# Optimization experiments

Measured on AMD Instinct MI355X. Metric: run time of the kernel, lower is better.

Reference implementation:

```python
import jax, jax.numpy as jnp
import numpy as np

N, D_IN, D_HID, D_OUT = 100000, 128, 512, 256
EPS = 1e-5


def _kaiming_uniform(k, shape):
    # torch kaiming_uniform_(a=sqrt(5)) -> bound = sqrt(1/fan_in)
    fan_in = shape[1]
    bound = float(np.sqrt(1.0 / fan_in))
    return jax.random.uniform(k, shape, minval=-bound, maxval=bound, dtype=jnp.float32)


def setup_inputs() -> dict:
    key = jax.random.key(0)
    ks = jax.random.split(key, 10)
    in_set = jax.random.normal(ks[0], (N, D_IN), dtype=jnp.float32)
    matA0 = _kaiming_uniform(ks[1], (D_HID, D_IN))
    matB0 = _kaiming_uniform(ks[2], (D_HID, D_IN))
    matA1 = _kaiming_uniform(ks[3], (D_HID, D_HID))
    matB1 = _kaiming_uniform(ks[4], (D_HID, D_HID))
    matA2 = _kaiming_uniform(ks[5], (D_HID, D_HID))
    matB2 = _kaiming_uniform(ks[6], (D_HID, D_HID))
    ln_gamma = jnp.ones((D_HID,), dtype=jnp.float32)
    ln_beta = jnp.zeros((D_HID,), dtype=jnp.float32)
    out_bound = float(np.sqrt(1.0 / D_HID))
    out_w = jax.random.uniform(ks[7], (D_OUT, D_HID), minval=-out_bound, maxval=out_bound, dtype=jnp.float32)
    out_b = jax.random.uniform(ks[8], (D_OUT,), minval=-out_bound, maxval=out_bound, dtype=jnp.float32)
    return {"in_set": in_set, "matA0": matA0, "matB0": matB0, "matA1": matA1, "matB1": matB1,
            "matA2": matA2, "matB2": matB2, "ln_gamma": ln_gamma, "ln_beta": ln_beta,
            "out_w": out_w, "out_b": out_b}


def _layer(h, A, B, g, b):
    # f(x_i) = relu(LN(A x_i + B (sum_j x_j - x_i)))
    # vectorized: h @ (A-B)^T + total_sum @ B^T  (sum-minus-self identity)
    s = h.sum(axis=0)  # [d]
    h = h @ (A - B).T + s @ B.T  # [N, d_hid]
    mu = h.mean(axis=-1, keepdims=True)
    var = jnp.mean((h - mu) ** 2, axis=-1, keepdims=True)
    h = (h - mu) / jnp.sqrt(var + EPS) * g + b
    return jax.nn.relu(h)


def reference(in_set, matA0, matB0, matA1, matB1, matA2, matB2, ln_gamma, ln_beta, out_w, out_b):
    h = _layer(in_set, matA0, matB0, ln_gamma, ln_beta)
    h = _layer(h, matA1, matB1, ln_gamma, ln_beta)
    h = _layer(h, matA2, matB2, ln_gamma, ln_beta)
    h = h.max(axis=0)  # max-pool over set elements -> [d_hid]
    return h @ out_w.T + out_b  # [d_out]
```

## Files before the change

kernel.cpp:

```cpp
#include <hip/hip_runtime.h>
#include <hip/hip_bf16.h>

#define NPTS 100000
#define NPTS_PAD 100096
#define DHID 512
#define EPSV 1e-5f

typedef __attribute__((ext_vector_type(4))) float f32x4;

#define OFF_INBF   0UL
#define OFF_W0     12812288UL
#define OFF_W1     12877824UL
#define OFF_W2     13139968UL
#define OFF_C0     13402112UL
#define OFF_C1     13404160UL
#define OFF_C2     13406208UL
#define OFF_PARTS  13408256UL
#define OFF_PARTS2 16609280UL
#define OFF_PARTS3 16740352UL
#define OFF_H1     16756736UL
#define OFF_H2     68005888UL

typedef const __attribute__((address_space(1))) unsigned int* gp_t;
typedef __attribute__((address_space(3))) unsigned int* lp_t;

__device__ __forceinline__ void async_copy16(const void* g, void* l) {
    __builtin_amdgcn_global_load_lds((gp_t)g, (lp_t)l, 16, 0, 0);
}

__device__ __forceinline__ unsigned pack4_fp8(float a, float b, float c, float d) {
    unsigned v = (unsigned)__builtin_amdgcn_cvt_pk_fp8_f32(a, b, 0, false);
    v = (unsigned)__builtin_amdgcn_cvt_pk_fp8_f32(c, d, (int)v, true);
    return v;
}

__global__ __launch_bounds__(256) void cvt_pack_kernel(const float* __restrict__ in,
                                                       unsigned char* __restrict__ out) {
    long total = (long)NPTS * 2;
    long stride = (long)gridDim.x * blockDim.x;
    for (long idx = (long)blockIdx.x * blockDim.x + threadIdx.x; idx < total; idx += stride) {
        int kt = (int)(idx / NPTS);
        long r = idx - (long)kt * NPTS;
        const float* src = in + r * 128 + kt * 64;
        unsigned dw[16];
#pragma unroll
        for (int m = 0; m < 16; ++m)
            dw[m] = pack4_fp8(src[m], src[16 + m], src[32 + m], src[48 + m]);
        uint4* dst = (uint4*)(out + r * 128 + kt * 64);
#pragma unroll
        for (int j = 0; j < 4; ++j)
            dst[j] = make_uint4(dw[4 * j], dw[4 * j + 1], dw[4 * j + 2], dw[4 * j + 3]);
    }
}

__global__ __launch_bounds__(256) void wpack_all_kernel(const float* __restrict__ A0,
                                                        const float* __restrict__ B0,
                                                        const float* __restrict__ A1,
                                                        const float* __restrict__ B1,
                                                        const float* __restrict__ A2,
                                                        const float* __restrict__ B2,
                                                        unsigned long long* __restrict__ W0,
                                                        unsigned long long* __restrict__ W1,
                                                        unsigned long long* __restrict__ W2) {
    int idx = blockIdx.x * 256 + threadIdx.x;
    const float *A, *B; unsigned long long* W; int NK, u;
    if (idx < 8192)       { A = A0; B = B0; W = W0; NK = 2; u = idx; }
    else if (idx < 40960) { A = A1; B = B1; W = W1; NK = 8; u = idx - 8192; }
    else                  { A = A2; B = B2; W = W2; NK = 8; u = idx - 40960; if (u >= 32768) return; }
    int KD = NK * 64;
    int lane = u & 63;
    int rest = u >> 6;
    int s = rest & 1;
    int fn = (rest >> 1) & 7;
    int ks = (rest >> 4) % NK;
    int wv = (rest >> 4) / NK;
    int ln15 = lane & 15, lg = lane >> 4;
    int row = wv * 128 + fn * 16 + ln15;
    int c0 = s * 8 + lg * 2;
    const float* sa = A + (long)row * KD + ks * 64;
    const float* sb = B + (long)row * KD + ks * 64;
    unsigned lo = pack4_fp8(sa[c0] - sb[c0], sa[16 + c0] - sb[16 + c0],
                            sa[32 + c0] - sb[32 + c0], sa[48 + c0] - sb[48 + c0]);
    unsigned hi = pack4_fp8(sa[c0 + 1] - sb[c0 + 1], sa[17 + c0] - sb[17 + c0],
                            sa[33 + c0] - sb[33 + c0], sa[49 + c0] - sb[49 + c0]);
    W[u] = ((unsigned long long)hi << 32) | lo;
}

__global__ __launch_bounds__(256) void colsum_in_kernel(const float* __restrict__ in,
                                                        float* __restrict__ parts) {
    __shared__ float sh[256];
    int t = threadIdx.x, blk = blockIdx.x;
    int c = t & 127, half = t >> 7;
    long rbeg = (long)blk * 196 + half;
    long rend = (long)(blk + 1) * 196; if (rend > NPTS) rend = NPTS;
    float s = 0.f;
    for (long r = rbeg; r < rend; r += 2) s += in[r * 128 + c];
    sh[t] = s;
    __syncthreads();
    if (t < 128) parts[blk * 128 + t] = sh[t] + sh[t + 128];
}

__global__ void part_reduceW_kernel(const float* __restrict__ parts, int nparts, int width,
                                    int op, float* __restrict__ out) {
    int g = blockIdx.x, t = threadIdx.x;
    int chunk = (nparts + gridDim.x - 1) / gridDim.x;
    int b0 = g * chunk, b1 = b0 + chunk; if (b1 > nparts) b1 = nparts;
    float s = 0.f;
    for (int b = b0; b < b1; ++b) {
        float v = parts[(long)b * width + t];
        s = (op == 0) ? (s + v) : fmaxf(s, v);
    }
    out[(long)g * width + t] = s;
}

__global__ __launch_bounds__(64) void gemv_fold_kernel(const float* __restrict__ p3, int dsum,
                                                       const float* __restrict__ Bm,
                                                       const float* __restrict__ bias, int op,
                                                       float* __restrict__ out) {
    int j = blockIdx.x, t = threadIdx.x;
    float acc = 0.f;
    for (int d = t; d < dsum; d += 64) {
        float s = 0.f;
#pragma unroll
        for (int g = 0; g < 8; ++g) {
            float v = p3[(long)g * dsum + d];
            s = (op == 0) ? (s + v) : fmaxf(s, v);
        }
        acc += s * Bm[(long)j * dsum + d];
    }
#pragma unroll
    for (int m = 32; m >= 1; m >>= 1) acc += __shfl_down(acc, m);
    if (t == 0) out[j] = acc + (bias ? bias[j] : 0.0f);
}

template<int KD, bool STORE, int REDOP>
__global__ __launch_bounds__(256, 2)
void layer_kernel(const unsigned char* __restrict__ Xp, const unsigned long long* __restrict__ Wp,
                  const float* __restrict__ cvec, const float* __restrict__ gvec,
                  const float* __restrict__ bvec, unsigned char* __restrict__ Hout,
                  float* __restrict__ red_out) {
    static_assert(KD % 64 == 0, "");
    constexpr int NK = KD / 64;
    __shared__ __align__(128) char smem[NK * 4096];

    const int t = threadIdx.x;
    const int lane = t & 63;
    const int wv = t >> 6;
    const int ln15 = lane & 15;
    const int lg = lane >> 4;
    const long row0 = (long)blockIdx.x * 64;

    f32x4 acc[4][8];
#pragma unroll
    for (int i = 0; i < 4; ++i)
#pragma unroll
        for (int j = 0; j < 8; ++j) acc[i][j] = (f32x4){0.f, 0.f, 0.f, 0.f};

    const int sr = t >> 2;
    const int ss = t & 3;
    const char* Xsrc = (const char*)Xp + (row0 + sr) * KD + ((ss ^ ((sr >> 1) & 3)) * 16);
    auto stage_x = [&](int kt) {
        async_copy16(Xsrc + kt * 64, smem + kt * 4096 + t * 16);
    };

    stage_x(0);
    if (NK > 1) stage_x(1);
    if (NK > 2) stage_x(2);

#define RD8X(BASE, r, sub) (*(const long*)((BASE) + (r) * 64 + \
        (((((sub) * 2 + (lg >> 1)) ^ (((r) >> 1) & 3)) * 16) + (lg & 1) * 8)))

    const unsigned long long* Wq = Wp + (long)wv * (NK * 16) * 64 + lane;
#pragma unroll
    for (int ks = 0; ks < NK; ++ks) {
        if (ks < NK - 2)       asm volatile("s_waitcnt vmcnt(2)" ::: "memory");
        else if (ks == NK - 2) asm volatile("s_waitcnt vmcnt(1)" ::: "memory");
        else                   asm volatile("s_waitcnt vmcnt(0)" ::: "memory");
        __builtin_amdgcn_s_barrier();
        __builtin_amdgcn_sched_barrier(0);
        if (ks + 3 < NK) stage_x(ks + 3);

        const char* Xs = smem + ks * 4096;
        long a0[4], a1[4];
#pragma unroll
        for (int fm = 0; fm < 4; ++fm) {
            int r = fm * 16 + ln15;
            a0[fm] = RD8X(Xs, r, 0);
            a1[fm] = RD8X(Xs, r, 1);
        }
#pragma unroll
        for (int fn = 0; fn < 8; ++fn) {
            long w0 = (long)Wq[(ks * 16 + fn * 2 + 0) * 64];
            long w1 = (long)Wq[(ks * 16 + fn * 2 + 1) * 64];
#pragma unroll
            for (int fm = 0; fm < 4; ++fm)
                acc[fm][fn] = __builtin_amdgcn_mfma_f32_16x16x32_fp8_fp8(a0[fm], w0, acc[fm][fn], 0, 0, 0);
#pragma unroll
            for (int fm = 0; fm < 4; ++fm)
                acc[fm][fn] = __builtin_amdgcn_mfma_f32_16x16x32_fp8_fp8(a1[fm], w1, acc[fm][fn], 0, 0, 0);
        }
    }
#undef RD8X
    __syncthreads();

    float* lnred_s = (float*)smem;
    float* lnred_q = (float*)(smem + 1024);
    float* lnmv    = (float*)(smem + 2048);

    const int cbase = wv * 128 + ln15;
    float cv[8], gv[8], bv[8];
#pragma unroll
    for (int fn = 0; fn < 8; ++fn) {
        int col = cbase + fn * 16;
        cv[fn] = cvec[col]; gv[fn] = gvec[col]; bv[fn] = bvec[col];
    }

#pragma unroll
    for (int fm = 0; fm < 4; ++fm)
#pragma unroll
        for (int fn = 0; fn < 8; ++fn) acc[fm][fn] += cv[fn];

    float rs[16], rq[16];
#pragma unroll
    for (int fm = 0; fm < 4; ++fm)
#pragma unroll
        for (int j = 0; j < 4; ++j) {
            float s = 0.f, q = 0.f;
#pragma unroll
            for (int fn = 0; fn < 8; ++fn) {
                float x = acc[fm][fn][j];
                s += x; q += x * x;
            }
            rs[fm * 4 + j] = s; rq[fm * 4 + j] = q;
        }
#pragma unroll
    for (int m = 1; m < 16; m <<= 1)
#pragma unroll
        for (int i = 0; i < 16; ++i) {
            rs[i] += __shfl_xor(rs[i], m);
            rq[i] += __shfl_xor(rq[i], m);
        }
    if (ln15 == 0) {
#pragma unroll
        for (int fm = 0; fm < 4; ++fm)
#pragma unroll
            for (int j = 0; j < 4; ++j) {
                int row = fm * 16 + lg * 4 + j;
                lnred_s[row * 4 + wv] = rs[fm * 4 + j];
                lnred_q[row * 4 + wv] = rq[fm * 4 + j];
            }
    }
    __syncthreads();
    if (t < 64) {
        float s = lnred_s[t * 4] + lnred_s[t * 4 + 1] + lnred_s[t * 4 + 2] + lnred_s[t * 4 + 3];
        float q = lnred_q[t * 4] + lnred_q[t * 4 + 1] + lnred_q[t * 4 + 2] + lnred_q[t * 4 + 3];
        float mu = s * (1.0f / 512.0f);
        float var = q * (1.0f / 512.0f) - mu * mu;
        lnmv[t * 2] = mu;
        lnmv[t * 2 + 1] = rsqrtf(var + EPSV);
    }
    __syncthreads();

#pragma unroll
    for (int fm = 0; fm < 4; ++fm)
#pragma unroll
        for (int j = 0; j < 4; ++j) {
            int rloc = fm * 16 + lg * 4 + j;
            long rglob = row0 + rloc;
            bool ok = rglob < NPTS;
            float mu = lnmv[rloc * 2], rstd = lnmv[rloc * 2 + 1];
#pragma unroll
            for (int fn = 0; fn < 8; ++fn) {
                float y = fmaxf((acc[fm][fn][j] - mu) * rstd * gv[fn] + bv[fn], 0.0f);
                acc[fm][fn][j] = ok ? y : 0.0f;
            }
            if (STORE) {
                unsigned ulo = pack4_fp8(acc[fm][0][j], acc[fm][1][j], acc[fm][2][j], acc[fm][3][j]);
                unsigned uhi = pack4_fp8(acc[fm][4][j], acc[fm][5][j], acc[fm][6][j], acc[fm][7][j]);
                char* base = (char*)Hout + rglob * DHID + wv * 128 + ln15 * 4;
                *(unsigned*)(base) = ulo;
                *(unsigned*)(base + 64) = uhi;
            }
        }

    float cp[8];
#pragma unroll
    for (int fn = 0; fn < 8; ++fn) {
        float p = 0.f;
#pragma unroll
        for (int fm = 0; fm < 4; ++fm)
#pragma unroll
            for (int j = 0; j < 4; ++j) {
                float v = acc[fm][fn][j];
                p = (REDOP == 0) ? (p + v) : fmaxf(p, v);
            }
        cp[fn] = p;
    }
#pragma unroll
    for (int m = 16; m < 64; m <<= 1)
#pragma unroll
        for (int fn = 0; fn < 8; ++fn) {
            float o = __shfl_xor(cp[fn], m);
            cp[fn] = (REDOP == 0) ? (cp[fn] + o) : fmaxf(cp[fn], o);
        }
    if (lane < 16) {
#pragma unroll
        for (int fn = 0; fn < 8; ++fn)
            red_out[(long)blockIdx.x * 512 + wv * 128 + fn * 16 + lane] = cp[fn];
    }
}

extern "C" void kernel_launch(void* const* d_in, const int* in_sizes, int n_in,
                              void* d_out, int out_size, void* d_ws, size_t ws_size,
                              hipStream_t stream) {
    const float* in_set = (const float*)d_in[0];
    const float* A0 = (const float*)d_in[1];
    const float* B0 = (const float*)d_in[2];
    const float* A1 = (const float*)d_in[3];
    const float* B1 = (const float*)d_in[4];
    const float* A2 = (const float*)d_in[5];
    const float* B2 = (const float*)d_in[6];
    const float* ga = (const float*)d_in[7];
    const float* be = (const float*)d_in[8];
    const float* ow = (const float*)d_in[9];
    const float* ob = (const float*)d_in[10];
    float* outp = (float*)d_out;
    char* ws = (char*)d_ws;

    unsigned char* in_f8 = (unsigned char*)(ws + OFF_INBF);
    unsigned long long* W0p = (unsigned long long*)(ws + OFF_W0);
    unsigned long long* W1p = (unsigned long long*)(ws + OFF_W1);
    unsigned long long* W2p = (unsigned long long*)(ws + OFF_W2);
    float* c0 = (float*)(ws + OFF_C0);
    float* c1 = (float*)(ws + OFF_C1);
    float* c2 = (float*)(ws + OFF_C2);
    float* parts = (float*)(ws + OFF_PARTS);
    float* parts2 = (float*)(ws + OFF_PARTS2);
    float* parts3 = (float*)(ws + OFF_PARTS3);
    unsigned char* h1 = (unsigned char*)(ws + OFF_H1);
    unsigned char* h2 = (unsigned char*)(ws + OFF_H2);

    const int nblk = (NPTS + 63) / 64;

    cvt_pack_kernel<<<1024, 256, 0, stream>>>(in_set, in_f8);
    wpack_all_kernel<<<288, 256, 0, stream>>>(A0, B0, A1, B1, A2, B2, W0p, W1p, W2p);

    colsum_in_kernel<<<512, 256, 0, stream>>>(in_set, parts);
    part_reduceW_kernel<<<64, 128, 0, stream>>>(parts, 512, 128, 0, parts2);
    part_reduceW_kernel<<<8, 128, 0, stream>>>(parts2, 64, 128, 0, parts3);
    gemv_fold_kernel<<<512, 64, 0, stream>>>(parts3, 128, B0, nullptr, 0, c0);

    layer_kernel<128, true, 0><<<nblk, 256, 0, stream>>>(in_f8, W0p, c0, ga, be, h1, parts);
    part_reduceW_kernel<<<64, 512, 0, stream>>>(parts, nblk, 512, 0, parts2);
    part_reduceW_kernel<<<8, 512, 0, stream>>>(parts2, 64, 512, 0, parts3);
    gemv_fold_kernel<<<512, 64, 0, stream>>>(parts3, 512, B1, nullptr, 0, c1);

    layer_kernel<512, true, 0><<<nblk, 256, 0, stream>>>(h1, W1p, c1, ga, be, h2, parts);
    part_reduceW_kernel<<<64, 512, 0, stream>>>(parts, nblk, 512, 0, parts2);
    part_reduceW_kernel<<<8, 512, 0, stream>>>(parts2, 64, 512, 0, parts3);
    gemv_fold_kernel<<<512, 64, 0, stream>>>(parts3, 512, B2, nullptr, 0, c2);

    layer_kernel<512, false, 1><<<nblk, 256, 0, stream>>>(h2, W2p, c2, ga, be, nullptr, parts);
    part_reduceW_kernel<<<64, 512, 0, stream>>>(parts, nblk, 512, 1, parts2);
    part_reduceW_kernel<<<8, 512, 0, stream>>>(parts2, 64, 512, 1, parts3);
    gemv_fold_kernel<<<256, 64, 0, stream>>>(parts3, 512, ow, ob, 1, outp);
}
```

Measured before the change: 297.8 us.

## Stage all X tiles upfront and double-buffer weight fragments in registers

Issues every async copy of the 64-row X tile into shared memory up front, followed by one barrier, in place of the rolling three-stage pipeline with per-step vmcnt waits and barriers. Weight fragments are prefetched one k-step ahead into a two-slot register buffer, so global weight loads overlap the MFMAs of the current step. This removes per-iteration barriers and hides weight load latency, but the first MFMA now waits for the whole tile to arrive. The extra 32 longs of register buffer also raise register pressure and may reduce occupancy.

```diff
diff --git a/kernel.cpp b/kernel.cpp
--- a/kernel.cpp
+++ b/kernel.cpp
@@ -156,30 +156,31 @@
 #pragma unroll
         for (int j = 0; j < 8; ++j) acc[i][j] = (f32x4){0.f, 0.f, 0.f, 0.f};
 
-    const int sr = t >> 2;
-    const int ss = t & 3;
-    const char* Xsrc = (const char*)Xp + (row0 + sr) * KD + ((ss ^ ((sr >> 1) & 3)) * 16);
-    auto stage_x = [&](int kt) {
-        async_copy16(Xsrc + kt * 64, smem + kt * 4096 + t * 16);
-    };
-
-    stage_x(0);
-    if (NK > 1) stage_x(1);
-    if (NK > 2) stage_x(2);
+    {
+        const int sr = t >> 2;
+        const int ss = t & 3;
+        const char* Xsrc = (const char*)Xp + (row0 + sr) * KD + ((ss ^ ((sr >> 1) & 3)) * 16);
+#pragma unroll
+        for (int kt = 0; kt < NK; ++kt)
+            async_copy16(Xsrc + kt * 64, smem + kt * 4096 + t * 16);
+    }
+    __syncthreads();
 
 #define RD8X(BASE, r, sub) (*(const long*)((BASE) + (r) * 64 + \
         (((((sub) * 2 + (lg >> 1)) ^ (((r) >> 1) & 3)) * 16) + (lg & 1) * 8)))
 
     const unsigned long long* Wq = Wp + (long)wv * (NK * 16) * 64 + lane;
+    long wbuf[2][16];
+#pragma unroll
+    for (int f = 0; f < 16; ++f) wbuf[0][f] = (long)Wq[f * 64];
+
 #pragma unroll
     for (int ks = 0; ks < NK; ++ks) {
-        if (ks < NK - 2)       asm volatile("s_waitcnt vmcnt(2)" ::: "memory");
-        else if (ks == NK - 2) asm volatile("s_waitcnt vmcnt(1)" ::: "memory");
-        else                   asm volatile("s_waitcnt vmcnt(0)" ::: "memory");
-        __builtin_amdgcn_s_barrier();
-        __builtin_amdgcn_sched_barrier(0);
-        if (ks + 3 < NK) stage_x(ks + 3);
-
+        if (ks + 1 < NK) {
+#pragma unroll
+            for (int f = 0; f < 16; ++f)
+                wbuf[(ks + 1) & 1][f] = (long)Wq[((ks + 1) * 16 + f) * 64];
+        }
         const char* Xs = smem + ks * 4096;
         long a0[4], a1[4];
 #pragma unroll
@@ -190,14 +191,14 @@
         }
 #pragma unroll
         for (int fn = 0; fn < 8; ++fn) {
-            long w0 = (long)Wq[(ks * 16 + fn * 2 + 0) * 64];
-            long w1 = (long)Wq[(ks * 16 + fn * 2 + 1) * 64];
 #pragma unroll
             for (int fm = 0; fm < 4; ++fm)
-                acc[fm][fn] = __builtin_amdgcn_mfma_f32_16x16x32_fp8_fp8(a0[fm], w0, acc[fm][fn], 0, 0, 0);
+                acc[fm][fn] = __builtin_amdgcn_mfma_f32_16x16x32_fp8_fp8(
+                    a0[fm], wbuf[ks & 1][fn * 2 + 0], acc[fm][fn], 0, 0, 0);
 #pragma unroll
             for (int fm = 0; fm < 4; ++fm)
-                acc[fm][fn] = __builtin_amdgcn_mfma_f32_16x16x32_fp8_fp8(a1[fm], w1, acc[fm][fn], 0, 0, 0);
+                acc[fm][fn] = __builtin_amdgcn_mfma_f32_16x16x32_fp8_fp8(
+                    a1[fm], wbuf[ks & 1][fn * 2 + 1], acc[fm][fn], 0, 0, 0);
         }
     }
 #undef RD8X
```

Result: faster. 264.9 us (-11.1%).
